# Optimization experiments

Hardware: AMD Instinct MI355X
Metric: run time of the kernel (lower is better)

Reference implementation:

```python
import jax, jax.numpy as jnp
import numpy as np

DIM = 256
HEADS = 8
NX = NY = 48
RNG = 5
MAX_IDX = (RNG + 1) ** 2  # 36, padding token


def _make_tokens(nx, ny, rng):
    # Half-symmetric tokenization of 2D relative positions (Learnable_rel_pos_embedding.tokenize)
    xm, ym = np.meshgrid(np.arange(nx), np.arange(ny), indexing='ij')
    xm, ym = xm.ravel(), ym.ravel()
    dx = xm[None, :] - xm[:, None]
    dy = ym[None, :] - ym[:, None]
    tok = np.abs(dx) * (rng + 1) + np.abs(dy)
    tok[(np.abs(dx) > rng) | (np.abs(dy) > rng)] = MAX_IDX
    return tok.astype(np.int32)


def setup_inputs() -> dict:
    key = jax.random.key(0)
    ks = jax.random.split(key, 10)
    s = DIM ** -0.5
    x = jax.random.normal(ks[0], (1, DIM, NX, NY), dtype=jnp.float32)
    Wq = jax.random.normal(ks[1], (DIM, DIM), dtype=jnp.float32) * s
    bq = jax.random.normal(ks[2], (DIM,), dtype=jnp.float32) * 0.01
    Wk = jax.random.normal(ks[3], (DIM, DIM), dtype=jnp.float32) * s
    bk = jax.random.normal(ks[4], (DIM,), dtype=jnp.float32) * 0.01
    Wv = jax.random.normal(ks[5], (DIM, DIM), dtype=jnp.float32) * s
    bv = jax.random.normal(ks[6], (DIM,), dtype=jnp.float32) * 0.01
    Wp = jax.random.normal(ks[7], (DIM, DIM), dtype=jnp.float32) * s
    bp = jax.random.normal(ks[8], (DIM,), dtype=jnp.float32) * 0.01
    emb = jax.random.normal(ks[9], (MAX_IDX + 1, HEADS), dtype=jnp.float32) * 0.02
    tokens = jnp.asarray(_make_tokens(NX, NY, RNG))  # (N, N) int32
    return dict(x=x, Wq=Wq, bq=bq, Wk=Wk, bk=bk, Wv=Wv, bv=bv,
                Wp=Wp, bp=bp, emb=emb, tokens=tokens)


def reference(x, Wq, bq, Wk, bk, Wv, bv, Wp, bp, emb, tokens):
    B, C, nx, ny = x.shape
    H = emb.shape[1]
    hd = C // H
    N = nx * ny
    scale = hd ** -0.5

    def conv1x1(W, b, t):
        return (jnp.einsum('oc,bcxy->boxy', W, t) + b[None, :, None, None])

    # Q/K/V as 1x1 convs, split into heads: (B, H, hd, N)
    q = conv1x1(Wq, bq, x).reshape(B, H, hd, N)
    k = conv1x1(Wk, bk, x).reshape(B, H, hd, N)
    v = conv1x1(Wv, bv, x).reshape(B, H, hd, N)

    # attn_method=2: scores = scale*QK^T + relative positional bias
    scores = jnp.einsum('bhdn,bhdm->bhnm', q, k) * scale  # (B, H, N, N)

    # pos_type=5: embedding lookup over half-symmetric relative-position tokens
    pad = emb.shape[0] - 1
    emb_masked = emb.at[pad].set(0.0)  # padding_idx row is zero
    pe = emb_masked[tokens]            # (N, N, H)
    scores = scores + jnp.transpose(pe, (2, 0, 1))[None]

    attn = jax.nn.softmax(scores, axis=-1)
    out = jnp.einsum('bhnm,bhdm->bhdn', attn, v).reshape(B, C, nx, ny)
    out = conv1x1(Wp, bp, out)
    return out
```

## Files before the change

kernel.cpp:

```cpp
#include <hip/hip_runtime.h>

#define NN 2304
#define CC 256
#define HH 8
#define HD 32
#define NYY 48
#define SCALE 0.17677669529663687f

typedef __bf16 bf16_t;
typedef __bf16 bf8v __attribute__((ext_vector_type(8)));
typedef __bf16 bf4v __attribute__((ext_vector_type(4)));
typedef float f4v __attribute__((ext_vector_type(4)));

__device__ __forceinline__ f4v mfma16(bf8v a, bf8v b, f4v c) {
    return __builtin_amdgcn_mfma_f32_16x16x32_bf16(a, b, c, 0, 0, 0);
}

__global__ __launch_bounds__(256) void k_pre(
    const float* __restrict__ x, bf16_t* __restrict__ xT,
    const float* __restrict__ Wq, const float* __restrict__ Wk,
    const float* __restrict__ Wv, const float* __restrict__ Wp,
    bf16_t* __restrict__ Wb) {
    const int b = blockIdx.x;
    const int t = threadIdx.x;
    if (b < 288) {
        __shared__ float tile[64][33];
        const int c0 = (b & 7) * 32;
        const int n0 = (b >> 3) * 64;
        const int n = t & 63, cb = t >> 6;
#pragma unroll
        for (int cc = 0; cc < 8; cc++) {
            int c = cc * 4 + cb;
            tile[n][c] = x[(size_t)(c0 + c) * NN + n0 + n];
        }
        __syncthreads();
        const int c = t & 31, nb = t >> 5;
#pragma unroll
        for (int nn = 0; nn < 8; nn++) {
            int n2 = nn * 8 + nb;
            xT[(size_t)(n0 + n2) * CC + c0 + c] = (bf16_t)tile[n2][c];
        }
    } else {
        const int wb = b - 288;
        const int matid = wb >> 5;
        const float* src = (matid == 0) ? Wq : (matid == 1) ? Wk : (matid == 2) ? Wv : Wp;
        const int base = (wb & 31) * 2048 + t * 8;
        float4 a = *(const float4*)(src + base);
        float4 c = *(const float4*)(src + base + 4);
        bf8v o;
        o[0] = (bf16_t)a.x; o[1] = (bf16_t)a.y; o[2] = (bf16_t)a.z; o[3] = (bf16_t)a.w;
        o[4] = (bf16_t)c.x; o[5] = (bf16_t)c.y; o[6] = (bf16_t)c.z; o[7] = (bf16_t)c.w;
        *(bf8v*)(Wb + (size_t)matid * 65536 + base) = o;
    }
}

__global__ __launch_bounds__(256) void k_proj_qkv(
    const bf16_t* __restrict__ Wb,
    const float* __restrict__ bq, const float* __restrict__ bk,
    const float* __restrict__ bv,
    const bf16_t* __restrict__ xT,
    bf16_t* __restrict__ Qt, bf16_t* __restrict__ Kt, bf16_t* __restrict__ Vd) {
    const int mat = blockIdx.z;
    const bf16_t* W = Wb + (size_t)mat * 65536;
    const float* bias = (mat == 0) ? bq : (mat == 1) ? bk : bv;
    const int n0 = blockIdx.x * 32;
    const int o0 = blockIdx.y * 64;
    const int lane = threadIdx.x & 63;
    const int wave = threadIdx.x >> 6;
    const int l15 = lane & 15;
    const int quad = lane >> 4;
    const int orow = o0 + wave * 16;

    f4v acc0 = {0.f, 0.f, 0.f, 0.f}, acc1 = {0.f, 0.f, 0.f, 0.f};
#pragma unroll
    for (int k0 = 0; k0 < CC; k0 += 32) {
        bf8v af = *(const bf8v*)(W + (size_t)(orow + l15) * CC + k0 + quad * 8);
        bf8v b0 = *(const bf8v*)(xT + (size_t)(n0 + l15) * CC + k0 + quad * 8);
        bf8v b1 = *(const bf8v*)(xT + (size_t)(n0 + 16 + l15) * CC + k0 + quad * 8);
        acc0 = mfma16(af, b0, acc0);
        acc1 = mfma16(af, b1, acc1);
    }

#pragma unroll
    for (int r = 0; r < 4; r++) {
        const int o = orow + quad * 4 + r;
        const float bo = bias[o];
#pragma unroll
        for (int nb = 0; nb < 2; nb++) {
            const int n = n0 + nb * 16 + l15;
            float v = (nb ? acc1[r] : acc0[r]) + bo;
            if (mat == 2) {
                Vd[(size_t)o * NN + n] = (bf16_t)v;
            } else {
                int h = o >> 5, d = o & 31;
                bf16_t* dst = (mat == 0) ? Qt : Kt;
                float vv = (mat == 0) ? v * SCALE : v;
                dst[(size_t)h * NN * HD + (size_t)n * HD + d] = (bf16_t)vv;
            }
        }
    }
}

template <int NITER>
__global__ __launch_bounds__(256, 8) void k_attn_split(
    const bf16_t* __restrict__ Qt, const bf16_t* __restrict__ Kt,
    const bf16_t* __restrict__ Vd, const float* __restrict__ emb,
    float* __restrict__ pO, float* __restrict__ pl) {
    __shared__ float lds_emb[40];
    __shared__ bf16_t lds_p[4][16 * 32];
    const int h = blockIdx.x & 7;
    const int qt = blockIdx.x >> 3;
    const int sidx = blockIdx.y;
    const int t = threadIdx.x;
    if (t < 37) lds_emb[t] = (t < 36) ? emb[t * HH + h] : 0.0f;
    __syncthreads();

    const int wave = t >> 6, lane = t & 63;
    const int l15 = lane & 15, quad = lane >> 4;
    const int qg0 = qt * 64 + wave * 16;
    const bf16_t* Qh = Qt + (size_t)h * NN * HD;
    const bf16_t* Kh = Kt + (size_t)h * NN * HD;
    const bf16_t* Vh = Vd + (size_t)h * HD * NN;

    const bf8v aq = *(const bf8v*)(Qh + (size_t)(qg0 + l15) * HD + quad * 8);

    int xi[4], yi[4];
#pragma unroll
    for (int r = 0; r < 4; r++) {
        int qi = qg0 + quad * 4 + r;
        xi[r] = qi / NYY;
        yi[r] = qi - xi[r] * NYY;
    }

    const int k_begin = sidx * (NITER * 32);
    int kj0 = k_begin + l15;
    int xj0 = kj0 / NYY, yj0 = kj0 - xj0 * NYY;
    int yj1 = yj0 + 16, xj1 = xj0;
    if (yj1 >= NYY) { yj1 -= NYY; xj1++; }

    f4v o0 = {0.f, 0.f, 0.f, 0.f}, o1 = {0.f, 0.f, 0.f, 0.f};
    const f4v z = {0.f, 0.f, 0.f, 0.f};
    float lsum[4] = {0.f, 0.f, 0.f, 0.f};
    bf16_t* plds = &lds_p[wave][0];

    bf8v kf0 = *(const bf8v*)(Kh + (size_t)(k_begin + l15) * HD + quad * 8);
    bf8v kf1 = *(const bf8v*)(Kh + (size_t)(k_begin + 16 + l15) * HD + quad * 8);
    bf8v vf0 = *(const bf8v*)(Vh + (size_t)l15 * NN + k_begin + quad * 8);
    bf8v vf1 = *(const bf8v*)(Vh + (size_t)(16 + l15) * NN + k_begin + quad * 8);

#pragma unroll 1
    for (int it = 0; it < NITER; ++it) {
        const int kb = k_begin + it * 32;
        const int nkb = (it + 1 < NITER) ? kb + 32 : k_begin;
        bf8v nkf0 = *(const bf8v*)(Kh + (size_t)(nkb + l15) * HD + quad * 8);
        bf8v nkf1 = *(const bf8v*)(Kh + (size_t)(nkb + 16 + l15) * HD + quad * 8);
        bf8v nvf0 = *(const bf8v*)(Vh + (size_t)l15 * NN + nkb + quad * 8);
        bf8v nvf1 = *(const bf8v*)(Vh + (size_t)(16 + l15) * NN + nkb + quad * 8);

        f4v s0 = mfma16(aq, kf0, z);
        f4v s1 = mfma16(aq, kf1, z);
#pragma unroll
        for (int r = 0; r < 4; r++) {
            int dx = xi[r] - xj0; dx = dx < 0 ? -dx : dx;
            int dy = yi[r] - yj0; dy = dy < 0 ? -dy : dy;
            int tok = (dx > 5 || dy > 5) ? 36 : dx * 6 + dy;
            float p = __expf(s0[r] + lds_emb[tok]);
            lsum[r] += p;
            plds[(quad * 4 + r) * 32 + l15] = (bf16_t)p;
        }
#pragma unroll
        for (int r = 0; r < 4; r++) {
            int dx = xi[r] - xj1; dx = dx < 0 ? -dx : dx;
            int dy = yi[r] - yj1; dy = dy < 0 ? -dy : dy;
            int tok = (dx > 5 || dy > 5) ? 36 : dx * 6 + dy;
            float p = __expf(s1[r] + lds_emb[tok]);
            lsum[r] += p;
            plds[(quad * 4 + r) * 32 + 16 + l15] = (bf16_t)p;
        }
        bf8v ap = *(const bf8v*)(plds + l15 * 32 + quad * 8);
        o0 = mfma16(ap, vf0, o0);
        o1 = mfma16(ap, vf1, o1);
        kf0 = nkf0; kf1 = nkf1; vf0 = nvf0; vf1 = nvf1;
        yj0 += 32; if (yj0 >= NYY) { yj0 -= NYY; xj0++; }
        yj1 += 32; if (yj1 >= NYY) { yj1 -= NYY; xj1++; }
    }

    float* pO_s = pO + ((size_t)sidx * HH + h) * NN * HD;
    float* pl_s = pl + ((size_t)sidx * HH + h) * NN;
#pragma unroll
    for (int r = 0; r < 4; r++) {
        float v = lsum[r];
#pragma unroll
        for (int m = 1; m < 16; m <<= 1) v += __shfl_xor(v, m, 64);
        int row = qg0 + quad * 4 + r;
        pO_s[(size_t)row * HD + l15] = o0[r];
        pO_s[(size_t)row * HD + 16 + l15] = o1[r];
        if (l15 == 0) pl_s[row] = v;
    }
}

__global__ __launch_bounds__(256) void k_reduce(
    const float* __restrict__ pO, const float* __restrict__ pl,
    bf16_t* __restrict__ Yt, int S) {
    const int e4 = blockIdx.x * 256 + threadIdx.x;
    const int h = e4 / (NN * HD / 4);
    const int rem = e4 - h * (NN * HD / 4);
    const int q = rem >> 3;
    const int d = (rem & 7) * 4;
    float4 so = {0.f, 0.f, 0.f, 0.f};
    float sl = 0.f;
    for (int s = 0; s < S; s++) {
        const float4 v = *(const float4*)(pO + ((size_t)s * HH + h) * NN * HD + (size_t)q * HD + d);
        so.x += v.x; so.y += v.y; so.z += v.z; so.w += v.w;
        sl += pl[((size_t)s * HH + h) * NN + q];
    }
    const float inv = 1.0f / sl;
    bf4v o;
    o[0] = (bf16_t)(so.x * inv); o[1] = (bf16_t)(so.y * inv);
    o[2] = (bf16_t)(so.z * inv); o[3] = (bf16_t)(so.w * inv);
    *(bf4v*)(Yt + (size_t)q * CC + h * HD + d) = o;
}

__global__ __launch_bounds__(512) void k_proj_out(
    const bf16_t* __restrict__ Wb, const float* __restrict__ bp,
    const bf16_t* __restrict__ Yt, float* __restrict__ out) {
    __shared__ float red[4 * 16 * 32];
    const bf16_t* W = Wb + (size_t)3 * 65536;
    const int n0 = blockIdx.x * 32;
    const int o0 = blockIdx.y * 64;
    const int t = threadIdx.x;
    const int lane = t & 63;
    const int wave = t >> 6;
    const int og = wave & 3;
    const int kg = wave >> 2;
    const int l15 = lane & 15;
    const int quad = lane >> 4;
    const int orow = o0 + og * 16;

    f4v acc0 = {0.f, 0.f, 0.f, 0.f}, acc1 = {0.f, 0.f, 0.f, 0.f};
#pragma unroll
    for (int ki = 0; ki < 4; ki++) {
        const int k0 = kg * 128 + ki * 32;
        bf8v af = *(const bf8v*)(W + (size_t)(orow + l15) * CC + k0 + quad * 8);
        bf8v b0 = *(const bf8v*)(Yt + (size_t)(n0 + l15) * CC + k0 + quad * 8);
        bf8v b1 = *(const bf8v*)(Yt + (size_t)(n0 + 16 + l15) * CC + k0 + quad * 8);
        acc0 = mfma16(af, b0, acc0);
        acc1 = mfma16(af, b1, acc1);
    }

    float* rg = red + og * 512;
    if (kg == 1) {
#pragma unroll
        for (int r = 0; r < 4; r++) {
            rg[(quad * 4 + r) * 32 + l15] = acc0[r];
            rg[(quad * 4 + r) * 32 + 16 + l15] = acc1[r];
        }
    }
    __syncthreads();
    if (kg == 0) {
#pragma unroll
        for (int r = 0; r < 4; r++) {
            const int o = orow + quad * 4 + r;
            const float bo = bp[o];
            out[(size_t)o * NN + n0 + l15] =
                acc0[r] + rg[(quad * 4 + r) * 32 + l15] + bo;
            out[(size_t)o * NN + n0 + 16 + l15] =
                acc1[r] + rg[(quad * 4 + r) * 32 + 16 + l15] + bo;
        }
    }
}

extern "C" void kernel_launch(void* const* d_in, const int* in_sizes, int n_in,
                              void* d_out, int out_size, void* d_ws, size_t ws_size,
                              hipStream_t stream) {
    const float* x   = (const float*)d_in[0];
    const float* Wq  = (const float*)d_in[1];
    const float* bq  = (const float*)d_in[2];
    const float* Wk  = (const float*)d_in[3];
    const float* bk  = (const float*)d_in[4];
    const float* Wv  = (const float*)d_in[5];
    const float* bv  = (const float*)d_in[6];
    const float* Wp  = (const float*)d_in[7];
    const float* bp  = (const float*)d_in[8];
    const float* emb = (const float*)d_in[9];
    float* out = (float*)d_out;

    bf16_t* xT = (bf16_t*)d_ws;
    bf16_t* Qt = xT + (size_t)NN * CC;
    bf16_t* Kt = Qt + (size_t)NN * CC;
    bf16_t* Vd = Kt + (size_t)NN * CC;
    bf16_t* Yt = Vd + (size_t)NN * CC;
    bf16_t* Wb = Yt + (size_t)NN * CC;
    float*  pO = (float*)(Wb + (size_t)4 * CC * CC);

    const size_t base_bytes = (size_t)5 * NN * CC * 2 + (size_t)4 * CC * CC * 2;
    const size_t per_split = (size_t)HH * NN * HD * 4 + (size_t)HH * NN * 4;
    int S = 1;
    if (base_bytes + 8 * per_split <= ws_size) S = 8;
    else if (base_bytes + 4 * per_split <= ws_size) S = 4;
    else if (base_bytes + 2 * per_split <= ws_size) S = 2;
    float* pl = pO + (size_t)S * HH * NN * HD;

    hipLaunchKernelGGL(k_pre, dim3(288 + 128), dim3(256), 0, stream,
                       x, xT, Wq, Wk, Wv, Wp, Wb);
    hipLaunchKernelGGL(k_proj_qkv, dim3(72, 4, 3), dim3(256), 0, stream,
                       Wb, bq, bk, bv, xT, Qt, Kt, Vd);
    switch (S) {
        case 8: hipLaunchKernelGGL((k_attn_split<9>),  dim3(288, 8), dim3(256), 0, stream, Qt, Kt, Vd, emb, pO, pl); break;
        case 4: hipLaunchKernelGGL((k_attn_split<18>), dim3(288, 4), dim3(256), 0, stream, Qt, Kt, Vd, emb, pO, pl); break;
        case 2: hipLaunchKernelGGL((k_attn_split<36>), dim3(288, 2), dim3(256), 0, stream, Qt, Kt, Vd, emb, pO, pl); break;
        default: hipLaunchKernelGGL((k_attn_split<72>), dim3(288, 1), dim3(256), 0, stream, Qt, Kt, Vd, emb, pO, pl); break;
    }
    hipLaunchKernelGGL(k_reduce, dim3((HH * NN * HD) / 1024), dim3(256), 0, stream,
                       pO, pl, Yt, S);
    hipLaunchKernelGGL(k_proj_out, dim3(72, 4), dim3(512), 0, stream, Wb, bp, Yt, out);
}
```

Before: 154.9 us.

## Precompute byte token table and exp(emb), transpose MFMA to drop LDS P staging

The pre-kernel now builds a per-pair uint8 relative-position token table (N×N bytes) and a per-head table of exp(emb), so the attention loop multiplies exp(score) by a looked-up factor instead of computing dx/dy tokens and adding the bias. The score MFMA operands are swapped so P comes out in register layout ready to feed the PV MFMA directly, removing the LDS round trip for P and the per-row shuffle reductions. Token bytes are prefetched two iterations ahead and V is loaded as two 4-wide halves to match the new layout. In exchange, the attention kernel reads an extra ~5 MB token table from global memory, and occupancy hints are lowered.

```diff
diff --git a/kernel.cpp b/kernel.cpp
--- a/kernel.cpp
+++ b/kernel.cpp
@@ -20,7 +20,8 @@
     const float* __restrict__ x, bf16_t* __restrict__ xT,
     const float* __restrict__ Wq, const float* __restrict__ Wk,
     const float* __restrict__ Wv, const float* __restrict__ Wp,
-    bf16_t* __restrict__ Wb) {
+    bf16_t* __restrict__ Wb, const float* __restrict__ emb,
+    unsigned char* __restrict__ tok8, float* __restrict__ ebt) {
     const int b = blockIdx.x;
     const int t = threadIdx.x;
     if (b < 288) {
@@ -40,7 +41,7 @@
             int n2 = nn * 8 + nb;
             xT[(size_t)(n0 + n2) * CC + c0 + c] = (bf16_t)tile[n2][c];
         }
-    } else {
+    } else if (b < 416) {
         const int wb = b - 288;
         const int matid = wb >> 5;
         const float* src = (matid == 0) ? Wq : (matid == 1) ? Wk : (matid == 2) ? Wv : Wp;
@@ -51,6 +52,35 @@
         o[0] = (bf16_t)a.x; o[1] = (bf16_t)a.y; o[2] = (bf16_t)a.z; o[3] = (bf16_t)a.w;
         o[4] = (bf16_t)c.x; o[5] = (bf16_t)c.y; o[6] = (bf16_t)c.z; o[7] = (bf16_t)c.w;
         *(bf8v*)(Wb + (size_t)matid * 65536 + base) = o;
+    } else if (b == 416) {
+        for (int i = t; i < 8 * 37; i += 256) {
+            int hh = i / 37, tk = i - hh * 37;
+            ebt[hh * 37 + tk] = (tk < 36) ? __expf(emb[tk * HH + hh]) : 1.0f;
+        }
+    } else {
+        const int e = (b - 417) * 256 + t;
+        const int qq = e / 144;
+        const int kk = (e - qq * 144) * 16;
+        const int xi = qq / NYY, yi = qq - xi * NYY;
+        const int xz = kk / NYY, yz = kk - xz * NYY;
+        int dx = xi - xz; dx = dx < 0 ? -dx : dx;
+        const bool xoob = dx > 5;
+        const int dx6 = dx * 6;
+        unsigned int w[4];
+#pragma unroll
+        for (int g = 0; g < 4; g++) {
+            unsigned int acc = 0;
+#pragma unroll
+            for (int j = 0; j < 4; j++) {
+                int yj = yz + g * 4 + j;
+                int dy = yi - yj; dy = dy < 0 ? -dy : dy;
+                int tok = (xoob || dy > 5) ? 36 : dx6 + dy;
+                acc |= (unsigned)tok << (j * 8);
+            }
+            w[g] = acc;
+        }
+        uint4 wv = {w[0], w[1], w[2], w[3]};
+        *(uint4*)(tok8 + (size_t)qq * NN + kk) = wv;
     }
 }
 
@@ -102,101 +132,109 @@
 }
 
 template <int NITER>
-__global__ __launch_bounds__(256, 8) void k_attn_split(
+__global__ __launch_bounds__(256, 4) void k_attn_split(
     const bf16_t* __restrict__ Qt, const bf16_t* __restrict__ Kt,
-    const bf16_t* __restrict__ Vd, const float* __restrict__ emb,
-    float* __restrict__ pO, float* __restrict__ pl) {
-    __shared__ float lds_emb[40];
-    __shared__ bf16_t lds_p[4][16 * 32];
+    const bf16_t* __restrict__ Vd, const unsigned char* __restrict__ tok8,
+    const float* __restrict__ ebt, float* __restrict__ pO,
+    float* __restrict__ pl) {
     const int h = blockIdx.x & 7;
     const int qt = blockIdx.x >> 3;
     const int sidx = blockIdx.y;
     const int t = threadIdx.x;
-    if (t < 37) lds_emb[t] = (t < 36) ? emb[t * HH + h] : 0.0f;
-    __syncthreads();
-
     const int wave = t >> 6, lane = t & 63;
     const int l15 = lane & 15, quad = lane >> 4;
     const int qg0 = qt * 64 + wave * 16;
+    const int q = qg0 + l15;
+
     const bf16_t* Qh = Qt + (size_t)h * NN * HD;
     const bf16_t* Kh = Kt + (size_t)h * NN * HD;
-    const bf16_t* Vh = Vd + (size_t)h * HD * NN;
-
-    const bf8v aq = *(const bf8v*)(Qh + (size_t)(qg0 + l15) * HD + quad * 8);
-
-    int xi[4], yi[4];
-#pragma unroll
-    for (int r = 0; r < 4; r++) {
-        int qi = qg0 + quad * 4 + r;
-        xi[r] = qi / NYY;
-        yi[r] = qi - xi[r] * NYY;
-    }
-
+    const bf16_t* v0p = Vd + (size_t)h * HD * NN + (size_t)l15 * NN;
+    const bf16_t* v1p = v0p + (size_t)16 * NN;
+    const float* eh = ebt + h * 37;
+    const unsigned char* tr = tok8 + (size_t)q * NN + quad * 4;
+
+    const bf8v aq = *(const bf8v*)(Qh + (size_t)q * HD + quad * 8);
     const int k_begin = sidx * (NITER * 32);
-    int kj0 = k_begin + l15;
-    int xj0 = kj0 / NYY, yj0 = kj0 - xj0 * NYY;
-    int yj1 = yj0 + 16, xj1 = xj0;
-    if (yj1 >= NYY) { yj1 -= NYY; xj1++; }
-
-    f4v o0 = {0.f, 0.f, 0.f, 0.f}, o1 = {0.f, 0.f, 0.f, 0.f};
-    const f4v z = {0.f, 0.f, 0.f, 0.f};
-    float lsum[4] = {0.f, 0.f, 0.f, 0.f};
-    bf16_t* plds = &lds_p[wave][0];
 
     bf8v kf0 = *(const bf8v*)(Kh + (size_t)(k_begin + l15) * HD + quad * 8);
     bf8v kf1 = *(const bf8v*)(Kh + (size_t)(k_begin + 16 + l15) * HD + quad * 8);
-    bf8v vf0 = *(const bf8v*)(Vh + (size_t)l15 * NN + k_begin + quad * 8);
-    bf8v vf1 = *(const bf8v*)(Vh + (size_t)(16 + l15) * NN + k_begin + quad * 8);
+    bf4v va0 = *(const bf4v*)(v0p + k_begin + quad * 4);
+    bf4v vb0 = *(const bf4v*)(v0p + k_begin + 16 + quad * 4);
+    bf4v va1 = *(const bf4v*)(v1p + k_begin + quad * 4);
+    bf4v vb1 = *(const bf4v*)(v1p + k_begin + 16 + quad * 4);
+    bf8v vf0 = __builtin_shufflevector(va0, vb0, 0, 1, 2, 3, 4, 5, 6, 7);
+    bf8v vf1 = __builtin_shufflevector(va1, vb1, 0, 1, 2, 3, 4, 5, 6, 7);
+
+    uint2 tka, tkb;
+    tka.x = *(const unsigned int*)(tr + k_begin);
+    tka.y = *(const unsigned int*)(tr + k_begin + 16);
+    {
+        const int kb1 = (NITER > 1) ? k_begin + 32 : k_begin;
+        tkb.x = *(const unsigned int*)(tr + kb1);
+        tkb.y = *(const unsigned int*)(tr + kb1 + 16);
+    }
+    float eb[8];
+#pragma unroll
+    for (int j = 0; j < 4; j++) eb[j] = eh[(tka.x >> (8 * j)) & 0xff];
+#pragma unroll
+    for (int j = 0; j < 4; j++) eb[4 + j] = eh[(tka.y >> (8 * j)) & 0xff];
+
+    const f4v z = {0.f, 0.f, 0.f, 0.f};
+    f4v o0 = z, o1 = z;
+    float lsum = 0.f;
 
 #pragma unroll 1
     for (int it = 0; it < NITER; ++it) {
-        const int kb = k_begin + it * 32;
-        const int nkb = (it + 1 < NITER) ? kb + 32 : k_begin;
-        bf8v nkf0 = *(const bf8v*)(Kh + (size_t)(nkb + l15) * HD + quad * 8);
-        bf8v nkf1 = *(const bf8v*)(Kh + (size_t)(nkb + 16 + l15) * HD + quad * 8);
-        bf8v nvf0 = *(const bf8v*)(Vh + (size_t)l15 * NN + nkb + quad * 8);
-        bf8v nvf1 = *(const bf8v*)(Vh + (size_t)(16 + l15) * NN + nkb + quad * 8);
-
-        f4v s0 = mfma16(aq, kf0, z);
-        f4v s1 = mfma16(aq, kf1, z);
+        const int kb1 = k_begin + ((it + 1 < NITER) ? (it + 1) * 32 : 0);
+        const int kb2 = k_begin + ((it + 2 < NITER) ? (it + 2) * 32 : 0);
+        bf8v nk0 = *(const bf8v*)(Kh + (size_t)(kb1 + l15) * HD + quad * 8);
+        bf8v nk1 = *(const bf8v*)(Kh + (size_t)(kb1 + 16 + l15) * HD + quad * 8);
+        bf4v na0 = *(const bf4v*)(v0p + kb1 + quad * 4);
+        bf4v nb0 = *(const bf4v*)(v0p + kb1 + 16 + quad * 4);
+        bf4v na1 = *(const bf4v*)(v1p + kb1 + quad * 4);
+        bf4v nb1 = *(const bf4v*)(v1p + kb1 + 16 + quad * 4);
+        uint2 tkc;
+        tkc.x = *(const unsigned int*)(tr + kb2);
+        tkc.y = *(const unsigned int*)(tr + kb2 + 16);
+        float ebn[8];
+#pragma unroll
+        for (int j = 0; j < 4; j++) ebn[j] = eh[(tkb.x >> (8 * j)) & 0xff];
+#pragma unroll
+        for (int j = 0; j < 4; j++) ebn[4 + j] = eh[(tkb.y >> (8 * j)) & 0xff];
+
+        f4v s0 = mfma16(kf0, aq, z);
+        f4v s1 = mfma16(kf1, aq, z);
+
+        float p[8];
 #pragma unroll
         for (int r = 0; r < 4; r++) {
-            int dx = xi[r] - xj0; dx = dx < 0 ? -dx : dx;
-            int dy = yi[r] - yj0; dy = dy < 0 ? -dy : dy;
-            int tok = (dx > 5 || dy > 5) ? 36 : dx * 6 + dy;
-            float p = __expf(s0[r] + lds_emb[tok]);
-            lsum[r] += p;
-            plds[(quad * 4 + r) * 32 + l15] = (bf16_t)p;
-        }
-#pragma unroll
-        for (int r = 0; r < 4; r++) {
-            int dx = xi[r] - xj1; dx = dx < 0 ? -dx : dx;
-            int dy = yi[r] - yj1; dy = dy < 0 ? -dy : dy;
-            int tok = (dx > 5 || dy > 5) ? 36 : dx * 6 + dy;
-            float p = __expf(s1[r] + lds_emb[tok]);
-            lsum[r] += p;
-            plds[(quad * 4 + r) * 32 + 16 + l15] = (bf16_t)p;
-        }
-        bf8v ap = *(const bf8v*)(plds + l15 * 32 + quad * 8);
-        o0 = mfma16(ap, vf0, o0);
-        o1 = mfma16(ap, vf1, o1);
-        kf0 = nkf0; kf1 = nkf1; vf0 = nvf0; vf1 = nvf1;
-        yj0 += 32; if (yj0 >= NYY) { yj0 -= NYY; xj0++; }
-        yj1 += 32; if (yj1 >= NYY) { yj1 -= NYY; xj1++; }
-    }
+            p[r] = __expf(s0[r]) * eb[r];
+            p[4 + r] = __expf(s1[r]) * eb[4 + r];
+        }
+#pragma unroll
+        for (int j = 0; j < 8; j++) lsum += p[j];
+        bf8v pb;
+#pragma unroll
+        for (int j = 0; j < 8; j++) pb[j] = (bf16_t)p[j];
+
+        o0 = mfma16(vf0, pb, o0);
+        o1 = mfma16(vf1, pb, o1);
+
+        kf0 = nk0; kf1 = nk1;
+        vf0 = __builtin_shufflevector(na0, nb0, 0, 1, 2, 3, 4, 5, 6, 7);
+        vf1 = __builtin_shufflevector(na1, nb1, 0, 1, 2, 3, 4, 5, 6, 7);
+        tka = tkb; tkb = tkc;
+#pragma unroll
+        for (int j = 0; j < 8; j++) eb[j] = ebn[j];
+    }
+
+    lsum += __shfl_xor(lsum, 16, 64);
+    lsum += __shfl_xor(lsum, 32, 64);
 
     float* pO_s = pO + ((size_t)sidx * HH + h) * NN * HD;
-    float* pl_s = pl + ((size_t)sidx * HH + h) * NN;
-#pragma unroll
-    for (int r = 0; r < 4; r++) {
-        float v = lsum[r];
-#pragma unroll
-        for (int m = 1; m < 16; m <<= 1) v += __shfl_xor(v, m, 64);
-        int row = qg0 + quad * 4 + r;
-        pO_s[(size_t)row * HD + l15] = o0[r];
-        pO_s[(size_t)row * HD + 16 + l15] = o1[r];
-        if (l15 == 0) pl_s[row] = v;
-    }
+    *(f4v*)(pO_s + (size_t)q * HD + quad * 4) = o0;
+    *(f4v*)(pO_s + (size_t)q * HD + 16 + quad * 4) = o1;
+    if (quad == 0) pl[((size_t)sidx * HH + h) * NN + q] = lsum;
 }
 
 __global__ __launch_bounds__(256) void k_reduce(
@@ -291,9 +329,16 @@
     bf16_t* Vd = Kt + (size_t)NN * CC;
     bf16_t* Yt = Vd + (size_t)NN * CC;
     bf16_t* Wb = Yt + (size_t)NN * CC;
-    float*  pO = (float*)(Wb + (size_t)4 * CC * CC);
-
-    const size_t base_bytes = (size_t)5 * NN * CC * 2 + (size_t)4 * CC * CC * 2;
+    unsigned char* tok8 = (unsigned char*)(Wb + (size_t)4 * CC * CC);
+    float* ebt = (float*)(tok8 + (size_t)NN * NN);
+    float* pO;
+    {
+        size_t off = (size_t)((char*)(ebt + 8 * 37) - (char*)d_ws);
+        off = (off + 15) & ~(size_t)15;
+        pO = (float*)((char*)d_ws + off);
+    }
+
+    const size_t base_bytes = (size_t)((char*)pO - (char*)d_ws);
     const size_t per_split = (size_t)HH * NN * HD * 4 + (size_t)HH * NN * 4;
     int S = 1;
     if (base_bytes + 8 * per_split <= ws_size) S = 8;
@@ -301,15 +346,15 @@
     else if (base_bytes + 2 * per_split <= ws_size) S = 2;
     float* pl = pO + (size_t)S * HH * NN * HD;
 
-    hipLaunchKernelGGL(k_pre, dim3(288 + 128), dim3(256), 0, stream,
-                       x, xT, Wq, Wk, Wv, Wp, Wb);
+    hipLaunchKernelGGL(k_pre, dim3(417 + 1296), dim3(256), 0, stream,
+                       x, xT, Wq, Wk, Wv, Wp, Wb, emb, tok8, ebt);
     hipLaunchKernelGGL(k_proj_qkv, dim3(72, 4, 3), dim3(256), 0, stream,
                        Wb, bq, bk, bv, xT, Qt, Kt, Vd);
     switch (S) {
-        case 8: hipLaunchKernelGGL((k_attn_split<9>),  dim3(288, 8), dim3(256), 0, stream, Qt, Kt, Vd, emb, pO, pl); break;
-        case 4: hipLaunchKernelGGL((k_attn_split<18>), dim3(288, 4), dim3(256), 0, stream, Qt, Kt, Vd, emb, pO, pl); break;
-        case 2: hipLaunchKernelGGL((k_attn_split<36>), dim3(288, 2), dim3(256), 0, stream, Qt, Kt, Vd, emb, pO, pl); break;
-        default: hipLaunchKernelGGL((k_attn_split<72>), dim3(288, 1), dim3(256), 0, stream, Qt, Kt, Vd, emb, pO, pl); break;
+        case 8: hipLaunchKernelGGL((k_attn_split<9>),  dim3(288, 8), dim3(256), 0, stream, Qt, Kt, Vd, tok8, ebt, pO, pl); break;
+        case 4: hipLaunchKernelGGL((k_attn_split<18>), dim3(288, 4), dim3(256), 0, stream, Qt, Kt, Vd, tok8, ebt, pO, pl); break;
+        case 2: hipLaunchKernelGGL((k_attn_split<36>), dim3(288, 2), dim3(256), 0, stream, Qt, Kt, Vd, tok8, ebt, pO, pl); break;
+        default: hipLaunchKernelGGL((k_attn_split<72>), dim3(288, 1), dim3(256), 0, stream, Qt, Kt, Vd, tok8, ebt, pO, pl); break;
     }
     hipLaunchKernelGGL(k_reduce, dim3((HH * NN * HD) / 1024), dim3(256), 0, stream,
                        pO, pl, Yt, S);
```

Result: slower. 194.1 us (+25.3%).
